# Performance work log

Hardware: AMD Instinct MI355X
Metric: run time of the kernel (lower is better)

## Reference

```python
import jax, jax.numpy as jnp
import numpy as np
from jax import lax

T, B, INP, HS, OUT = 256, 128, 1024, 1024, 1024


def setup_inputs() -> dict:
    key = jax.random.key(0)
    ks = jax.random.split(key, 7)
    s = 1.0 / np.sqrt(HS)  # scale params to keep tanh out of deep saturation
    return {
        "data": jax.random.normal(ks[0], (T, B, INP), jnp.float32),
        "W_ih": jax.random.normal(ks[1], (INP, HS), jnp.float32) * s,
        "W_hh": jax.random.normal(ks[2], (HS, HS), jnp.float32) * s,
        "b_i": jax.random.normal(ks[3], (HS,), jnp.float32) * s,
        "b_h": jax.random.normal(ks[4], (HS,), jnp.float32) * s,
        "W_out": jax.random.normal(ks[5], (OUT, HS), jnp.float32) * s,
        "b_out": jax.random.normal(ks[6], (OUT,), jnp.float32) * s,
    }


def reference(data, W_ih, W_hh, b_i, b_h, W_out, b_out):
    # Elman RNN: h_{t+1} = tanh(x_t @ W_ih + b_i + h_t @ W_hh + b_h)
    bias = b_i + b_h
    h0 = jnp.zeros((data.shape[1], W_hh.shape[0]), data.dtype)

    def step(h, x_t):
        h_new = jnp.tanh(x_t @ W_ih + h @ W_hh + bias)
        return h_new, None

    h_final, _ = lax.scan(step, h0, data)
    # nn.Linear: out = h @ W_out.T + b_out
    return h_final @ W_out.T + b_out
```

## Files before the change

### kernel.cpp

```cpp
#include <hip/hip_runtime.h>
#include <hip/hip_bf16.h>
#include <math.h>


typedef __attribute__((ext_vector_type(8))) short bf16x8;
typedef __attribute__((ext_vector_type(4))) float f32x4;
typedef __attribute__((ext_vector_type(4))) unsigned int u32x4;
typedef __attribute__((ext_vector_type(2))) unsigned int u32x2;

#define TT 256
#define BB 128
#define HS 1024
#define H_ELEMS (BB * HS)
#define POISON32 0xAAAAAAAAu

__device__ __forceinline__ short f2bf(float x) {
  __hip_bfloat16 b = __float2bfloat16(x);
  return *reinterpret_cast<short*>(&b);
}
__device__ __forceinline__ float bf2f(unsigned short s) {
  unsigned int u = ((unsigned int)s) << 16;
  float f;
  __builtin_memcpy(&f, &u, 4);
  return f;
}
__device__ __forceinline__ float fast_exp2(float x) {
#if __has_builtin(__builtin_amdgcn_exp2f)
  return __builtin_amdgcn_exp2f(x);
#else
  return exp2f(x);
#endif
}
__device__ __forceinline__ float fast_rcp(float x) {
#if __has_builtin(__builtin_amdgcn_rcpf)
  return __builtin_amdgcn_rcpf(x);
#else
  return 1.0f / x;
#endif
}
__device__ __forceinline__ float fast_tanh(float x) {
  float xc = fminf(fmaxf(x, -9.0f), 9.0f);
  float e = fast_exp2(2.8853900817779268f * xc);
  return (e - 1.0f) * fast_rcp(e + 1.0f);
}

__device__ __forceinline__ void mall_load_b128(u32x4* dst, const void* p) {
  asm volatile("global_load_dwordx4 %0, %1, off sc0 sc1" : "=v"(*dst) : "v"(p) : "memory");
}
__device__ __forceinline__ void mall_store_b64(void* p, u32x2 v) {
  asm volatile("global_store_dwordx2 %0, %1, off sc0 sc1" :: "v"(p), "v"(v) : "memory");
}
__device__ __forceinline__ void mall_store_b32(void* p, unsigned v) {
  asm volatile("global_store_dword %0, %1, off sc0 sc1" :: "v"(p), "v"(v) : "memory");
}
__device__ __forceinline__ unsigned mall_poll_b32(const void* p) {
  unsigned v;
  asm volatile("global_load_dword %0, %1, off sc0 sc1" : "=v"(v) : "v"(p) : "memory");
  asm volatile("s_waitcnt vmcnt(0)" : "+v"(v));
  return v;
}
__device__ __forceinline__ void wait_vm0() {
  asm volatile("s_waitcnt vmcnt(0)" ::: "memory");
}
#define TIE4(d)                                                         \
  asm volatile("s_waitcnt vmcnt(0)"                                     \
               : "+v"(d[0]), "+v"(d[1]), "+v"(d[2]), "+v"(d[3]))

__global__ __launch_bounds__(256) void cvt_data(const float* __restrict__ src,
                                                __hip_bfloat16* __restrict__ dst) {
  size_t i = ((size_t)blockIdx.x * 256 + threadIdx.x) * 8;
  f32x4 a = *reinterpret_cast<const f32x4*>(src + i);
  f32x4 b = *reinterpret_cast<const f32x4*>(src + i + 4);
  bf16x8 v;
  v[0] = f2bf(a[0]); v[1] = f2bf(a[1]); v[2] = f2bf(a[2]); v[3] = f2bf(a[3]);
  v[4] = f2bf(b[0]); v[5] = f2bf(b[1]); v[6] = f2bf(b[2]); v[7] = f2bf(b[3]);
  *reinterpret_cast<bf16x8*>(dst + i) = v;
}

__global__ __launch_bounds__(256) void cvt_tr2(const float* __restrict__ s0,
                                               __hip_bfloat16* __restrict__ d0,
                                               const float* __restrict__ s1,
                                               __hip_bfloat16* __restrict__ d1) {
  __shared__ __hip_bfloat16 T[64][72];
  const float* src = blockIdx.z ? s1 : s0;
  __hip_bfloat16* dst = blockIdx.z ? d1 : d0;
  const int tid = threadIdx.x;
  const int k0 = blockIdx.y * 64, n0 = blockIdx.x * 64;
  const int r = tid >> 4, c4 = (tid & 15) * 4;
#pragma unroll
  for (int p = 0; p < 4; ++p) {
    int kk = r + p * 16;
    f32x4 v = *reinterpret_cast<const f32x4*>(src + (size_t)(k0 + kk) * 1024 + n0 + c4);
#pragma unroll
    for (int j = 0; j < 4; ++j) T[c4 + j][kk] = __float2bfloat16(v[j]);
  }
  __syncthreads();
  const int rr = tid >> 3, u = tid & 7;
#pragma unroll
  for (int p = 0; p < 2; ++p) {
    int R = rr + p * 32;
    *reinterpret_cast<bf16x8*>(dst + (size_t)(n0 + R) * 1024 + k0 + u * 8) =
        *reinterpret_cast<const bf16x8*>(&T[R][u * 8]);
  }
}

template <bool ABF>
__global__ __launch_bounds__(512, 1) void gemm_xw5(
    const void* __restrict__ Ain,
    const __hip_bfloat16* __restrict__ Bt,
    const float* __restrict__ b_i,
    const float* __restrict__ b_h,
    __hip_bfloat16* __restrict__ P) {
  __shared__ __hip_bfloat16 As[256][72];
  __shared__ __hip_bfloat16 Bs[128][72];

  const int tid = threadIdx.x;
  const int m0 = blockIdx.y * 256, n0 = blockIdx.x * 128;
  const int wave = tid >> 6, lane = tid & 63;
  const int wm = wave & 3, wn = wave >> 2;
  const int quad = lane >> 4, l16 = lane & 15;
  const int sr = tid >> 3, su = tid & 7;

  f32x4 acc[4][4] = {};

  for (int k0 = 0; k0 < 1024; k0 += 64) {
    __syncthreads();
#pragma unroll
    for (int p = 0; p < 4; ++p) {
      int row = sr + p * 64;
      bf16x8 av;
      if (ABF) {
        av = *reinterpret_cast<const bf16x8*>(
            (const __hip_bfloat16*)Ain + (size_t)(m0 + row) * 1024 + k0 + su * 8);
      } else {
        const float* ap = (const float*)Ain + (size_t)(m0 + row) * 1024 + k0 + su * 8;
        f32x4 x = *reinterpret_cast<const f32x4*>(ap);
        f32x4 y = *reinterpret_cast<const f32x4*>(ap + 4);
        av[0] = f2bf(x[0]); av[1] = f2bf(x[1]); av[2] = f2bf(x[2]); av[3] = f2bf(x[3]);
        av[4] = f2bf(y[0]); av[5] = f2bf(y[1]); av[6] = f2bf(y[2]); av[7] = f2bf(y[3]);
      }
      *reinterpret_cast<bf16x8*>(&As[row][su * 8]) = av;
    }
#pragma unroll
    for (int p = 0; p < 2; ++p) {
      int row = sr + p * 64;
      bf16x8 bv = *reinterpret_cast<const bf16x8*>(
          Bt + (size_t)(n0 + row) * 1024 + k0 + su * 8);
      *reinterpret_cast<bf16x8*>(&Bs[row][su * 8]) = bv;
    }
    __syncthreads();
#pragma unroll
    for (int kk = 0; kk < 2; ++kk) {
      bf16x8 af[4], bfr[4];
#pragma unroll
      for (int mi = 0; mi < 4; ++mi)
        af[mi] = *reinterpret_cast<const bf16x8*>(&As[wm * 64 + mi * 16 + l16][kk * 32 + quad * 8]);
#pragma unroll
      for (int ni = 0; ni < 4; ++ni)
        bfr[ni] = *reinterpret_cast<const bf16x8*>(&Bs[wn * 64 + ni * 16 + l16][kk * 32 + quad * 8]);
#pragma unroll
      for (int mi = 0; mi < 4; ++mi)
#pragma unroll
        for (int ni = 0; ni < 4; ++ni)
          acc[mi][ni] = __builtin_amdgcn_mfma_f32_16x16x32_bf16(af[mi], bfr[ni], acc[mi][ni], 0, 0, 0);
    }
  }

  float bias[4];
#pragma unroll
  for (int ni = 0; ni < 4; ++ni) {
    int col = n0 + wn * 64 + ni * 16 + l16;
    bias[ni] = b_i[col] + b_h[col];
  }
#pragma unroll
  for (int mi = 0; mi < 4; ++mi)
#pragma unroll
    for (int ni = 0; ni < 4; ++ni) {
      int row = m0 + wm * 64 + mi * 16 + quad * 4;
      int col = n0 + wn * 64 + ni * 16 + l16;
#pragma unroll
      for (int r = 0; r < 4; ++r)
        P[(size_t)(row + r) * 1024 + col] = __float2bfloat16(acc[mi][ni][r] + bias[ni]);
    }
}

__global__ __launch_bounds__(512, 1) void rnn_scan9b(
    const __hip_bfloat16* __restrict__ P,
    const __hip_bfloat16* __restrict__ W_hhT,
    __hip_bfloat16* __restrict__ hslots) {
  __shared__ __hip_bfloat16 Ht[2][16 * 1024];
  __shared__ __hip_bfloat16 Csw[8][16][20];

  const int tid = threadIdx.x;
  const int m = blockIdx.x & 7;
  const int ng = blockIdx.x >> 3;
  const int m0 = m * 16, n0 = ng * 128;

  const int wv = tid >> 6, lane = tid & 63;
  const int quad = lane >> 4, l16 = lane & 15;
  const int colloc = wv * 16 + l16;
  const int col = n0 + colloc;
  const int xorl = l16 & 7;
  const int r16 = tid >> 5;
  const int s32 = tid & 31;
  const int erow = lane >> 2, eseg = lane & 3;

  bf16x8 wreg[32];
#pragma unroll
  for (int wi = 0; wi < 32; ++wi)
    wreg[wi] = *reinterpret_cast<const bf16x8*>(
        W_hhT + (size_t)col * 1024 + wi * 32 + quad * 8);

  unsigned short pvA[4], pvB[4];
  {
    const __hip_bfloat16* Pt0 = P + (size_t)(m0 + quad * 4) * 1024 + col;
#pragma unroll
    for (int r = 0; r < 4; ++r)
      pvA[r] = *reinterpret_cast<const unsigned short*>(Pt0 + (size_t)r * 1024);
  }

  for (int t = 0; t < TT; ++t) {
    const __hip_bfloat16* hc = hslots + (size_t)t * H_ELEMS;
    __hip_bfloat16* hn = hslots + (size_t)(t + 1) * H_ELEMS;
    __hip_bfloat16* htb = Ht[t & 1];

    const char* src = (const char*)(hc + (size_t)(m0 + r16) * 1024) + s32 * 16;
    u32x4 d[4];
    {
      int g = 0;
      for (;;) {
        mall_load_b128(&d[0], src);
        mall_load_b128(&d[1], src + 512);
        mall_load_b128(&d[2], src + 1024);
        mall_load_b128(&d[3], src + 1536);
        TIE4(d);
        bool ok = true;
#pragma unroll
        for (int i = 0; i < 4; ++i)
#pragma unroll
          for (int w2 = 0; w2 < 4; ++w2)
            ok &= (d[i][w2] != POISON32);
        if (ok || ++g >= (1 << 14)) break;
      }
    }

    {
      int tn = (t + 1 < TT) ? t + 1 : TT - 1;
      const __hip_bfloat16* Ptn =
          P + (size_t)tn * H_ELEMS + (size_t)(m0 + quad * 4) * 1024 + col;
#pragma unroll
      for (int r = 0; r < 4; ++r)
        pvB[r] = *reinterpret_cast<const unsigned short*>(Ptn + (size_t)r * 1024);
    }

#pragma unroll
    for (int i = 0; i < 4; ++i) {
      int u = s32 + i * 32;
      int gp = u ^ (r16 & 7) ^ (u >> 4);
      *reinterpret_cast<u32x4*>(&htb[r16 * 1024 + gp * 8]) = d[i];
    }
    __syncthreads();

    f32x4 acc[4] = {{0.f, 0.f, 0.f, 0.f}, {0.f, 0.f, 0.f, 0.f},
                    {0.f, 0.f, 0.f, 0.f}, {0.f, 0.f, 0.f, 0.f}};
#pragma unroll
    for (int c = 0; c < 8; ++c) {
#pragma unroll
      for (int j = 0; j < 4; ++j) {
        int G = c * 16 + j * 4 + quad;
        int gp = G ^ xorl ^ c;
        bf16x8 af = *reinterpret_cast<const bf16x8*>(&htb[l16 * 1024 + gp * 8]);
        acc[j] = __builtin_amdgcn_mfma_f32_16x16x32_bf16(af, wreg[c * 4 + j], acc[j], 0, 0, 0);
      }
    }

#pragma unroll
    for (int r = 0; r < 4; ++r) {
      float s = (acc[0][r] + acc[1][r]) + (acc[2][r] + acc[3][r]) + bf2f(pvA[r]);
      Csw[wv][quad * 4 + r][l16] = __float2bfloat16(fast_tanh(s));
    }
    {
      u32x2 val = *reinterpret_cast<const u32x2*>(&Csw[wv][erow][eseg * 4]);
      mall_store_b64(hn + (size_t)(m0 + erow) * 1024 + n0 + wv * 16 + eseg * 4, val);
    }

#pragma unroll
    for (int r = 0; r < 4; ++r) pvA[r] = pvB[r];
  }
  wait_vm0();
}

__global__ __launch_bounds__(512, 2) void rnn_scan7(
    const __hip_bfloat16* __restrict__ P,
    const float* __restrict__ W_hh,
    __hip_bfloat16* __restrict__ hbuf,
    unsigned* __restrict__ flags) {
  __shared__ __hip_bfloat16 Wt[32 * 1024];
  __shared__ __hip_bfloat16 Ht[16 * 1024];
  __shared__ __hip_bfloat16 Cs[16 * 132];

  const int tid = threadIdx.x;
  const int m = blockIdx.x & 7;
  const int ng = blockIdx.x >> 3;
  const int m0 = m * 16, n0 = ng * 128;

  const int wv = tid >> 6, lane = tid & 63;
  const int quad = lane >> 4, l16 = lane & 15;
  const int colloc = wv * 16 + l16;
  const int col = n0 + colloc;
  const int nl = (wv & 1) * 16 + l16;
  const int xorl = l16 & 7;
  const int r16 = tid >> 5;
  const int s32 = tid & 31;
  unsigned* gflags = flags + m * 8;

  bf16x8 wreg[32];
  for (int cch = 0; cch < 4; ++cch) {
    if (cch) __syncthreads();
    const int nb = n0 + cch * 32;
    for (int i = tid; i < 32 * 1024 / 4; i += 512) {
      int nq = i & 7, k = i >> 3;
      f32x4 v = *reinterpret_cast<const f32x4*>(W_hh + (size_t)k * 1024 + nb + nq * 4);
#pragma unroll
      for (int j = 0; j < 4; ++j) {
        int nll = nq * 4 + j;
        int sg = (k >> 3) ^ (nll & 7);
        Wt[nll * 1024 + sg * 8 + (k & 7)] = __float2bfloat16(v[j]);
      }
    }
    __syncthreads();
    if ((wv >> 1) == cch) {
#pragma unroll
      for (int wi = 0; wi < 32; ++wi) {
        int G = wi * 4 + quad;
        int sg = G ^ (nl & 7);
        wreg[wi] = *reinterpret_cast<const bf16x8*>(&Wt[nl * 1024 + sg * 8]);
      }
    }
  }
  __syncthreads();

  for (int t = 0; t < TT; ++t) {
    const __hip_bfloat16* hc = hbuf + (size_t)(t & 1) * H_ELEMS;
    __hip_bfloat16* hn = hbuf + (size_t)((t + 1) & 1) * H_ELEMS;

    const __hip_bfloat16* Pt =
        P + (size_t)t * H_ELEMS + (size_t)(m0 + quad * 4) * 1024 + col;
    unsigned short pv[4];
#pragma unroll
    for (int r = 0; r < 4; ++r)
      pv[r] = *reinterpret_cast<const unsigned short*>(Pt + (size_t)r * 1024);

    if (t > 0) {
      if (tid < 8) {
        const unsigned* fp = gflags + tid;
        int g = 0;
        while (mall_poll_b32(fp) < (unsigned)t && ++g < (1 << 18)) {}
      }
      __syncthreads();
    }

    {
      const char* src = (const char*)(hc + (size_t)(m0 + r16) * 1024) + s32 * 16;
      u32x4 d[4];
      mall_load_b128(&d[0], src);
      mall_load_b128(&d[1], src + 512);
      mall_load_b128(&d[2], src + 1024);
      mall_load_b128(&d[3], src + 1536);
      TIE4(d);
#pragma unroll
      for (int i = 0; i < 4; ++i) {
        int u = s32 + i * 32;
        int gp = u ^ (r16 & 7) ^ (u >> 4);
        *reinterpret_cast<u32x4*>(&Ht[r16 * 1024 + gp * 8]) = d[i];
      }
    }
    __syncthreads();

    f32x4 acc[4] = {{0.f, 0.f, 0.f, 0.f}, {0.f, 0.f, 0.f, 0.f},
                    {0.f, 0.f, 0.f, 0.f}, {0.f, 0.f, 0.f, 0.f}};
#pragma unroll
    for (int c = 0; c < 8; ++c) {
#pragma unroll
      for (int j = 0; j < 4; ++j) {
        int G = c * 16 + j * 4 + quad;
        int gp = G ^ xorl ^ c;
        bf16x8 af = *reinterpret_cast<const bf16x8*>(&Ht[l16 * 1024 + gp * 8]);
        acc[j] = __builtin_amdgcn_mfma_f32_16x16x32_bf16(af, wreg[c * 4 + j], acc[j], 0, 0, 0);
      }
    }

#pragma unroll
    for (int r = 0; r < 4; ++r) {
      float s = (acc[0][r] + acc[1][r]) + (acc[2][r] + acc[3][r]) + bf2f(pv[r]);
      Cs[(quad * 4 + r) * 132 + colloc] = __float2bfloat16(fast_tanh(s));
    }
    __syncthreads();
    {
      u32x2 val = *reinterpret_cast<const u32x2*>(&Cs[r16 * 132 + s32 * 4]);
      mall_store_b64(hn + (size_t)(m0 + r16) * 1024 + n0 + s32 * 4, val);
      wait_vm0();
    }
    __syncthreads();

    if (t != TT - 1 && tid == 0)
      mall_store_b32(gflags + ng, (unsigned)(t + 1));
  }
}

__global__ __launch_bounds__(256) void gemm_out(
    const __hip_bfloat16* __restrict__ h,
    const float* __restrict__ W_out,
    const float* __restrict__ b_out,
    float* __restrict__ out) {
  const int tid = threadIdx.x;
  const int wave = tid >> 6, lane = tid & 63;
  const int quad = lane >> 4, l16 = lane & 15;
  const int o = blockIdx.x * 64 + wave * 16 + l16;

  f32x4 acc[8] = {};
  for (int k0 = 0; k0 < 1024; k0 += 32) {
    f32x4 w0 = *reinterpret_cast<const f32x4*>(W_out + (size_t)o * 1024 + k0 + quad * 8);
    f32x4 w1 = *reinterpret_cast<const f32x4*>(W_out + (size_t)o * 1024 + k0 + quad * 8 + 4);
    bf16x8 bfr;
    bfr[0] = f2bf(w0[0]); bfr[1] = f2bf(w0[1]); bfr[2] = f2bf(w0[2]); bfr[3] = f2bf(w0[3]);
    bfr[4] = f2bf(w1[0]); bfr[5] = f2bf(w1[1]); bfr[6] = f2bf(w1[2]); bfr[7] = f2bf(w1[3]);
#pragma unroll
    for (int mi = 0; mi < 8; ++mi) {
      bf16x8 af = *reinterpret_cast<const bf16x8*>(h + (size_t)(mi * 16 + l16) * 1024 + k0 + quad * 8);
      acc[mi] = __builtin_amdgcn_mfma_f32_16x16x32_bf16(af, bfr, acc[mi], 0, 0, 0);
    }
  }
  const float bias = b_out[o];
#pragma unroll
  for (int mi = 0; mi < 8; ++mi)
#pragma unroll
    for (int r = 0; r < 4; ++r)
      out[(size_t)(mi * 16 + quad * 4 + r) * 1024 + o] = acc[mi][r] + bias;
}

extern "C" void kernel_launch(void* const* d_in, const int* in_sizes, int n_in,
                              void* d_out, int out_size, void* d_ws, size_t ws_size,
                              hipStream_t stream) {
  const float* data  = (const float*)d_in[0];
  const float* W_ih  = (const float*)d_in[1];
  const float* W_hh  = (const float*)d_in[2];
  const float* b_i   = (const float*)d_in[3];
  const float* b_h   = (const float*)d_in[4];
  const float* W_out = (const float*)d_in[5];
  const float* b_out = (const float*)d_in[6];
  float* out = (float*)d_out;

  char* ws = (char*)d_ws;
  const size_t OFF_P   = 0;
  const size_t OFF_H   = (size_t)TT * H_ELEMS * 2;
  const size_t OFF_FLG = OFF_H + 2 * H_ELEMS * 2;
  const size_t OFF_WT  = OFF_FLG + 1024;
  const size_t OFF_WH  = OFF_WT + 2u * 1024 * 1024;
  const size_t OFF_DB  = OFF_WH + 2u * 1024 * 1024;
  const size_t DB_B    = (size_t)TT * H_ELEMS * 2;

  const size_t SLOT_B  = (size_t)H_ELEMS * 2;
  const size_t SLOTS_B = (size_t)(TT + 1) * SLOT_B;
  const size_t OFF_S_SEP = OFF_DB + DB_B;
  const size_t NEED_SEP  = OFF_S_SEP + SLOTS_B;
  const size_t NEED_OVL  = OFF_DB + SLOTS_B;

  __hip_bfloat16* P     = (__hip_bfloat16*)(ws + OFF_P);
  __hip_bfloat16* hbuf  = (__hip_bfloat16*)(ws + OFF_H);
  unsigned* flags       = (unsigned*)(ws + OFF_FLG);
  __hip_bfloat16* W_ihT = (__hip_bfloat16*)(ws + OFF_WT);
  __hip_bfloat16* W_hhT = (__hip_bfloat16*)(ws + OFF_WH);
  __hip_bfloat16* dataB = (__hip_bfloat16*)(ws + OFF_DB);

  if (ws_size >= NEED_SEP) {
    __hip_bfloat16* slots = (__hip_bfloat16*)(ws + OFF_S_SEP);
    hipMemsetAsync(ws + OFF_S_SEP, 0, SLOT_B, stream);
    cvt_tr2<<<dim3(16, 16, 2), 256, 0, stream>>>(W_ih, W_ihT, W_hh, W_hhT);
    cvt_data<<<16384, 256, 0, stream>>>(data, dataB);
    gemm_xw5<true><<<dim3(8, 128), 512, 0, stream>>>(dataB, W_ihT, b_i, b_h, P);
    rnn_scan9b<<<64, 512, 0, stream>>>(P, W_hhT, slots);
    gemm_out<<<16, 256, 0, stream>>>(slots + (size_t)TT * H_ELEMS, W_out, b_out, out);
  } else if (ws_size >= NEED_OVL) {
    __hip_bfloat16* slots = (__hip_bfloat16*)(ws + OFF_DB);
    cvt_tr2<<<dim3(16, 16, 2), 256, 0, stream>>>(W_ih, W_ihT, W_hh, W_hhT);
    gemm_xw5<false><<<dim3(8, 128), 512, 0, stream>>>(data, W_ihT, b_i, b_h, P);
    hipMemsetAsync(ws + OFF_DB, 0, SLOT_B, stream);
    hipMemsetAsync(ws + OFF_DB + SLOT_B, 0xAA, SLOTS_B - SLOT_B, stream);
    rnn_scan9b<<<64, 512, 0, stream>>>(P, W_hhT, slots);
    gemm_out<<<16, 256, 0, stream>>>(slots + (size_t)TT * H_ELEMS, W_out, b_out, out);
  } else {
    hipMemsetAsync(ws + OFF_H, 0, 2 * H_ELEMS * 2 + 1024, stream);
    cvt_tr2<<<dim3(16, 16, 1), 256, 0, stream>>>(W_ih, W_ihT, W_ih, W_ihT);
    gemm_xw5<false><<<dim3(8, 128), 512, 0, stream>>>(data, W_ihT, b_i, b_h, P);
    rnn_scan7<<<64, 512, 0, stream>>>(P, W_hh, hbuf, flags);
    gemm_out<<<16, 256, 0, stream>>>(hbuf, W_out, b_out, out);
  }
}
```

Baseline: 980.1 us.

## Halve scan waves with two column tiles per wave and shrink GEMM tile

```diff
diff --git a/kernel.cpp b/kernel.cpp
--- a/kernel.cpp
+++ b/kernel.cpp
@@ -47,6 +47,9 @@
 __device__ __forceinline__ void mall_load_b128(u32x4* dst, const void* p) {
   asm volatile("global_load_dwordx4 %0, %1, off sc0 sc1" : "=v"(*dst) : "v"(p) : "memory");
 }
+__device__ __forceinline__ void mall_store_b128(void* p, u32x4 v) {
+  asm volatile("global_store_dwordx4 %0, %1, off sc0 sc1" :: "v"(p), "v"(v) : "memory");
+}
 __device__ __forceinline__ void mall_store_b64(void* p, u32x2 v) {
   asm volatile("global_store_dwordx2 %0, %1, off sc0 sc1" :: "v"(p), "v"(v) : "memory");
 }
@@ -65,6 +68,10 @@
 #define TIE4(d)                                                         \
   asm volatile("s_waitcnt vmcnt(0)"                                     \
                : "+v"(d[0]), "+v"(d[1]), "+v"(d[2]), "+v"(d[3]))
+#define TIE8(d)                                                         \
+  asm volatile("s_waitcnt vmcnt(0)"                                     \
+               : "+v"(d[0]), "+v"(d[1]), "+v"(d[2]), "+v"(d[3]),        \
+                 "+v"(d[4]), "+v"(d[5]), "+v"(d[6]), "+v"(d[7]))
 
 __global__ __launch_bounds__(256) void cvt_data(const float* __restrict__ src,
                                                 __hip_bfloat16* __restrict__ dst) {
@@ -105,19 +112,19 @@
 }
 
 template <bool ABF>
-__global__ __launch_bounds__(512, 1) void gemm_xw5(
+__global__ __launch_bounds__(256) void gemm_xw2(
     const void* __restrict__ Ain,
     const __hip_bfloat16* __restrict__ Bt,
     const float* __restrict__ b_i,
     const float* __restrict__ b_h,
     __hip_bfloat16* __restrict__ P) {
-  __shared__ __hip_bfloat16 As[256][72];
+  __shared__ __hip_bfloat16 As[128][72];
   __shared__ __hip_bfloat16 Bs[128][72];
 
   const int tid = threadIdx.x;
-  const int m0 = blockIdx.y * 256, n0 = blockIdx.x * 128;
+  const int m0 = blockIdx.y * 128, n0 = blockIdx.x * 128;
   const int wave = tid >> 6, lane = tid & 63;
-  const int wm = wave & 3, wn = wave >> 2;
+  const int wm = wave & 1, wn = wave >> 1;
   const int quad = lane >> 4, l16 = lane & 15;
   const int sr = tid >> 3, su = tid & 7;
 
@@ -127,7 +134,7 @@
     __syncthreads();
 #pragma unroll
     for (int p = 0; p < 4; ++p) {
-      int row = sr + p * 64;
+      int row = sr + p * 32;
       bf16x8 av;
       if (ABF) {
         av = *reinterpret_cast<const bf16x8*>(
@@ -140,10 +147,6 @@
         av[4] = f2bf(y[0]); av[5] = f2bf(y[1]); av[6] = f2bf(y[2]); av[7] = f2bf(y[3]);
       }
       *reinterpret_cast<bf16x8*>(&As[row][su * 8]) = av;
-    }
-#pragma unroll
-    for (int p = 0; p < 2; ++p) {
-      int row = sr + p * 64;
       bf16x8 bv = *reinterpret_cast<const bf16x8*>(
           Bt + (size_t)(n0 + row) * 1024 + k0 + su * 8);
       *reinterpret_cast<bf16x8*>(&Bs[row][su * 8]) = bv;
@@ -184,12 +187,12 @@
     }
 }
 
-__global__ __launch_bounds__(512, 1) void rnn_scan9b(
+__global__ __launch_bounds__(256, 1) void rnn_scan9c(
     const __hip_bfloat16* __restrict__ P,
     const __hip_bfloat16* __restrict__ W_hhT,
     __hip_bfloat16* __restrict__ hslots) {
   __shared__ __hip_bfloat16 Ht[2][16 * 1024];
-  __shared__ __hip_bfloat16 Csw[8][16][20];
+  __shared__ __align__(16) __hip_bfloat16 Csw[4][16][40];
 
   const int tid = threadIdx.x;
   const int m = blockIdx.x & 7;
@@ -198,25 +201,30 @@
 
   const int wv = tid >> 6, lane = tid & 63;
   const int quad = lane >> 4, l16 = lane & 15;
-  const int colloc = wv * 16 + l16;
-  const int col = n0 + colloc;
+  const int colA = n0 + wv * 32 + l16;
+  const int colB = colA + 16;
   const int xorl = l16 & 7;
-  const int r16 = tid >> 5;
-  const int s32 = tid & 31;
+  const int r16 = tid >> 4;
+  const int s16 = tid & 15;
   const int erow = lane >> 2, eseg = lane & 3;
 
-  bf16x8 wreg[32];
-#pragma unroll
-  for (int wi = 0; wi < 32; ++wi)
-    wreg[wi] = *reinterpret_cast<const bf16x8*>(
-        W_hhT + (size_t)col * 1024 + wi * 32 + quad * 8);
-
-  unsigned short pvA[4], pvB[4];
+  bf16x8 wregA[32], wregB[32];
+#pragma unroll
+  for (int wi = 0; wi < 32; ++wi) {
+    wregA[wi] = *reinterpret_cast<const bf16x8*>(
+        W_hhT + (size_t)colA * 1024 + wi * 32 + quad * 8);
+    wregB[wi] = *reinterpret_cast<const bf16x8*>(
+        W_hhT + (size_t)colB * 1024 + wi * 32 + quad * 8);
+  }
+
+  unsigned short pvA[8], pvB[8];
   {
-    const __hip_bfloat16* Pt0 = P + (size_t)(m0 + quad * 4) * 1024 + col;
-#pragma unroll
-    for (int r = 0; r < 4; ++r)
-      pvA[r] = *reinterpret_cast<const unsigned short*>(Pt0 + (size_t)r * 1024);
+    const __hip_bfloat16* Pt0 = P + (size_t)(m0 + quad * 4) * 1024;
+#pragma unroll
+    for (int r = 0; r < 4; ++r) {
+      pvA[r]     = *reinterpret_cast<const unsigned short*>(Pt0 + (size_t)r * 1024 + colA);
+      pvA[4 + r] = *reinterpret_cast<const unsigned short*>(Pt0 + (size_t)r * 1024 + colB);
+    }
   }
 
   for (int t = 0; t < TT; ++t) {
@@ -224,19 +232,23 @@
     __hip_bfloat16* hn = hslots + (size_t)(t + 1) * H_ELEMS;
     __hip_bfloat16* htb = Ht[t & 1];
 
-    const char* src = (const char*)(hc + (size_t)(m0 + r16) * 1024) + s32 * 16;
-    u32x4 d[4];
+    const char* src = (const char*)(hc + (size_t)(m0 + r16) * 1024) + s16 * 16;
+    u32x4 d[8];
     {
       int g = 0;
       for (;;) {
         mall_load_b128(&d[0], src);
-        mall_load_b128(&d[1], src + 512);
-        mall_load_b128(&d[2], src + 1024);
-        mall_load_b128(&d[3], src + 1536);
-        TIE4(d);
+        mall_load_b128(&d[1], src + 256);
+        mall_load_b128(&d[2], src + 512);
+        mall_load_b128(&d[3], src + 768);
+        mall_load_b128(&d[4], src + 1024);
+        mall_load_b128(&d[5], src + 1280);
+        mall_load_b128(&d[6], src + 1536);
+        mall_load_b128(&d[7], src + 1792);
+        TIE8(d);
         bool ok = true;
 #pragma unroll
-        for (int i = 0; i < 4; ++i)
+        for (int i = 0; i < 8; ++i)
 #pragma unroll
           for (int w2 = 0; w2 < 4; ++w2)
             ok &= (d[i][w2] != POISON32);
@@ -246,23 +258,26 @@
 
     {
       int tn = (t + 1 < TT) ? t + 1 : TT - 1;
-      const __hip_bfloat16* Ptn =
-          P + (size_t)tn * H_ELEMS + (size_t)(m0 + quad * 4) * 1024 + col;
-#pragma unroll
-      for (int r = 0; r < 4; ++r)
-        pvB[r] = *reinterpret_cast<const unsigned short*>(Ptn + (size_t)r * 1024);
-    }
-
-#pragma unroll
-    for (int i = 0; i < 4; ++i) {
-      int u = s32 + i * 32;
+      const __hip_bfloat16* Ptn = P + (size_t)tn * H_ELEMS + (size_t)(m0 + quad * 4) * 1024;
+#pragma unroll
+      for (int r = 0; r < 4; ++r) {
+        pvB[r]     = *reinterpret_cast<const unsigned short*>(Ptn + (size_t)r * 1024 + colA);
+        pvB[4 + r] = *reinterpret_cast<const unsigned short*>(Ptn + (size_t)r * 1024 + colB);
+      }
+    }
+
+#pragma unroll
+    for (int i = 0; i < 8; ++i) {
+      int u = s16 + i * 16;
       int gp = u ^ (r16 & 7) ^ (u >> 4);
       *reinterpret_cast<u32x4*>(&htb[r16 * 1024 + gp * 8]) = d[i];
     }
     __syncthreads();
 
-    f32x4 acc[4] = {{0.f, 0.f, 0.f, 0.f}, {0.f, 0.f, 0.f, 0.f},
-                    {0.f, 0.f, 0.f, 0.f}, {0.f, 0.f, 0.f, 0.f}};
+    f32x4 accA[4] = {{0.f, 0.f, 0.f, 0.f}, {0.f, 0.f, 0.f, 0.f},
+                     {0.f, 0.f, 0.f, 0.f}, {0.f, 0.f, 0.f, 0.f}};
+    f32x4 accB[4] = {{0.f, 0.f, 0.f, 0.f}, {0.f, 0.f, 0.f, 0.f},
+                     {0.f, 0.f, 0.f, 0.f}, {0.f, 0.f, 0.f, 0.f}};
 #pragma unroll
     for (int c = 0; c < 8; ++c) {
 #pragma unroll
@@ -270,22 +285,25 @@
         int G = c * 16 + j * 4 + quad;
         int gp = G ^ xorl ^ c;
         bf16x8 af = *reinterpret_cast<const bf16x8*>(&htb[l16 * 1024 + gp * 8]);
-        acc[j] = __builtin_amdgcn_mfma_f32_16x16x32_bf16(af, wreg[c * 4 + j], acc[j], 0, 0, 0);
+        accA[j] = __builtin_amdgcn_mfma_f32_16x16x32_bf16(af, wregA[c * 4 + j], accA[j], 0, 0, 0);
+        accB[j] = __builtin_amdgcn_mfma_f32_16x16x32_bf16(af, wregB[c * 4 + j], accB[j], 0, 0, 0);
       }
     }
 
 #pragma unroll
     for (int r = 0; r < 4; ++r) {
-      float s = (acc[0][r] + acc[1][r]) + (acc[2][r] + acc[3][r]) + bf2f(pvA[r]);
-      Csw[wv][quad * 4 + r][l16] = __float2bfloat16(fast_tanh(s));
+      float sA = (accA[0][r] + accA[1][r]) + (accA[2][r] + accA[3][r]) + bf2f(pvA[r]);
+      float sB = (accB[0][r] + accB[1][r]) + (accB[2][r] + accB[3][r]) + bf2f(pvA[4 + r]);
+      Csw[wv][quad * 4 + r][l16]      = __float2bfloat16(fast_tanh(sA));
+      Csw[wv][quad * 4 + r][16 + l16] = __float2bfloat16(fast_tanh(sB));
     }
     {
-      u32x2 val = *reinterpret_cast<const u32x2*>(&Csw[wv][erow][eseg * 4]);
-      mall_store_b64(hn + (size_t)(m0 + erow) * 1024 + n0 + wv * 16 + eseg * 4, val);
-    }
-
-#pragma unroll
-    for (int r = 0; r < 4; ++r) pvA[r] = pvB[r];
+      u32x4 val = *reinterpret_cast<const u32x4*>(&Csw[wv][erow][eseg * 8]);
+      mall_store_b128(hn + (size_t)(m0 + erow) * 1024 + n0 + wv * 32 + eseg * 8, val);
+    }
+
+#pragma unroll
+    for (int r = 0; r < 8; ++r) pvA[r] = pvB[r];
   }
   wait_vm0();
 }
@@ -478,21 +496,21 @@
     hipMemsetAsync(ws + OFF_S_SEP, 0, SLOT_B, stream);
     cvt_tr2<<<dim3(16, 16, 2), 256, 0, stream>>>(W_ih, W_ihT, W_hh, W_hhT);
     cvt_data<<<16384, 256, 0, stream>>>(data, dataB);
-    gemm_xw5<true><<<dim3(8, 128), 512, 0, stream>>>(dataB, W_ihT, b_i, b_h, P);
-    rnn_scan9b<<<64, 512, 0, stream>>>(P, W_hhT, slots);
+    gemm_xw2<true><<<dim3(8, 256), 256, 0, stream>>>(dataB, W_ihT, b_i, b_h, P);
+    rnn_scan9c<<<64, 256, 0, stream>>>(P, W_hhT, slots);
     gemm_out<<<16, 256, 0, stream>>>(slots + (size_t)TT * H_ELEMS, W_out, b_out, out);
   } else if (ws_size >= NEED_OVL) {
     __hip_bfloat16* slots = (__hip_bfloat16*)(ws + OFF_DB);
     cvt_tr2<<<dim3(16, 16, 2), 256, 0, stream>>>(W_ih, W_ihT, W_hh, W_hhT);
-    gemm_xw5<false><<<dim3(8, 128), 512, 0, stream>>>(data, W_ihT, b_i, b_h, P);
+    gemm_xw2<false><<<dim3(8, 256), 256, 0, stream>>>(data, W_ihT, b_i, b_h, P);
     hipMemsetAsync(ws + OFF_DB, 0, SLOT_B, stream);
     hipMemsetAsync(ws + OFF_DB + SLOT_B, 0xAA, SLOTS_B - SLOT_B, stream);
-    rnn_scan9b<<<64, 512, 0, stream>>>(P, W_hhT, slots);
+    rnn_scan9c<<<64, 256, 0, stream>>>(P, W_hhT, slots);
     gemm_out<<<16, 256, 0, stream>>>(slots + (size_t)TT * H_ELEMS, W_out, b_out, out);
   } else {
     hipMemsetAsync(ws + OFF_H, 0, 2 * H_ELEMS * 2 + 1024, stream);
     cvt_tr2<<<dim3(16, 16, 1), 256, 0, stream>>>(W_ih, W_ihT, W_ih, W_ihT);
-    gemm_xw5<false><<<dim3(8, 128), 512, 0, stream>>>(data, W_ihT, b_i, b_h, P);
+    gemm_xw2<false><<<dim3(8, 256), 256, 0, stream>>>(data, W_ihT, b_i, b_h, P);
     rnn_scan7<<<64, 512, 0, stream>>>(P, W_hh, hbuf, flags);
     gemm_out<<<16, 256, 0, stream>>>(hbuf, W_out, b_out, out);
   }
```

Result: slower. 1.366 ms (+39.3%).
